# Kernel optimization log

Measured on AMD Instinct MI355X. Metric: run time of the kernel, lower is better.

Reference implementation:

```python
import jax, jax.numpy as jnp
import numpy as np

N = 2048
HW = 36          # resized feature map
NBLK = 4         # n_H = n_V = 4
P = HW // NBLK   # 9x9 patches
C_ENC = 8        # encoder output channels
HD = 2           # ConvLSTM hidden dim
OUT_DIM = 24


def setup_inputs() -> dict:
    key = jax.random.key(0)
    ks = jax.random.split(key, 14)
    s = 0.05
    return {
        "color_feat": jax.random.normal(ks[0], (N, 32, HW, HW), jnp.float32),
        "geo_feat": jax.random.normal(ks[1], (N, 32, HW, HW), jnp.float32),
        # encoder: Conv2d(64,32,1) then Conv2d(32,8,1) -> 1x1 convs as matrices
        "enc_w1": jax.random.normal(ks[2], (32, 64), jnp.float32) * s,
        "enc_b1": jax.random.normal(ks[3], (32,), jnp.float32) * s,
        "enc_w2": jax.random.normal(ks[4], (C_ENC, 32), jnp.float32) * s,
        "enc_b2": jax.random.normal(ks[5], (C_ENC,), jnp.float32) * s,
        # ConvLSTM layer 1: in 8 + hidden 2 -> 4*hidden gates, 1x1 kernel
        "lstm_w1": jax.random.normal(ks[6], (4 * HD, C_ENC + HD), jnp.float32) * s,
        "lstm_b1": jax.random.normal(ks[7], (4 * HD,), jnp.float32) * s,
        # ConvLSTM layer 2: in 2 + hidden 2 -> 4*hidden gates
        "lstm_w2": jax.random.normal(ks[8], (4 * HD, HD + HD), jnp.float32) * s,
        "lstm_b2": jax.random.normal(ks[9], (4 * HD,), jnp.float32) * s,
        # LazyLinear(24) on flattened [N, 2*9*9]
        "out_w": jax.random.normal(ks[10], (OUT_DIM, HD * P * P), jnp.float32) * s,
        "out_b": jax.random.normal(ks[11], (OUT_DIM,), jnp.float32) * s,
    }


def _conv1x1(x, w, b):
    # x: [N,Cin,H,W], w: [Cout,Cin], b: [Cout]
    return jnp.einsum("nchw,oc->nohw", x, w) + b[None, :, None, None]


def _convlstm_layer(x_seq, w, b, hd):
    # x_seq: [T,N,Cin,h,w]; 1x1-kernel ConvLSTM layer, zero-initialized state
    T, n, _, hh, ww = x_seq.shape
    h0 = jnp.zeros((n, hd, hh, ww), x_seq.dtype)
    c0 = jnp.zeros((n, hd, hh, ww), x_seq.dtype)

    def cell(carry, x):
        h, c = carry
        cat = jnp.concatenate([x, h], axis=1)
        gates = jnp.einsum("nchw,gc->nghw", cat, w) + b[None, :, None, None]
        i, f, o, g = jnp.split(gates, 4, axis=1)
        c_next = jax.nn.sigmoid(f) * c + jax.nn.sigmoid(i) * jnp.tanh(g)
        h_next = jax.nn.sigmoid(o) * jnp.tanh(c_next)
        return (h_next, c_next), h_next

    (_, _), h_seq = jax.lax.scan(cell, (h0, c0), x_seq)
    return h_seq  # [T,N,hd,h,w]


def reference(color_feat, geo_feat, enc_w1, enc_b1, enc_w2, enc_b2,
              lstm_w1, lstm_b1, lstm_w2, lstm_b2, out_w, out_b):
    # concat features (already resized to 36x36) -> encoder (two 1x1 convs)
    all_feats = jnp.concatenate([color_feat, geo_feat], axis=1)  # [N,64,36,36]
    enc = _conv1x1(_conv1x1(all_feats, enc_w1, enc_b1), enc_w2, enc_b2)  # [N,8,36,36]

    n = enc.shape[0]
    # torch unfold over (C,H,W) -> [N, 16, C, 9, 9] ordered (h_block, w_block)
    patches = enc.reshape(n, C_ENC, NBLK, P, NBLK, P)
    patches = patches.transpose(0, 2, 4, 1, 3, 5).reshape(n, NBLK * NBLK, C_ENC, P, P)

    x_seq = patches.transpose(1, 0, 2, 3, 4)  # [T=16, N, 8, 9, 9]
    h1 = _convlstm_layer(x_seq, lstm_w1, lstm_b1, HD)   # [T,N,2,9,9]
    h2 = _convlstm_layer(h1, lstm_w2, lstm_b2, HD)      # [T,N,2,9,9]

    last = h2[-1]                       # [N,2,9,9] last timestep of last layer
    flat = last.reshape(n, -1)          # [N,162]
    return flat @ out_w.T + out_b       # [N,24]
```

## Files before the change

### kernel.cpp

```cpp
#include <hip/hip_runtime.h>
#include <cstddef>

#define HWDIM 36
#define PIX   1296
#define PIX4  324
#define CIN   64
#define CENC  8
#define HD    2
#define T_SEQ 16
#define PP    9
#define NPOS  81
#define FLATD 162
#define ODIM  24
#define BLOCK 384

__device__ __forceinline__ float sigm(float x) {
    return 1.f / (1.f + __expf(-x));
}
__device__ __forceinline__ float tanh_f(float x) {
    x = fminf(15.f, fmaxf(-15.f, x));
    float e = __expf(2.f * x);
    return (e - 1.f) / (e + 1.f);
}
__device__ __forceinline__ void fma4(float4& a, float w, const float4& v) {
    a.x = fmaf(w, v.x, a.x);
    a.y = fmaf(w, v.y, a.y);
    a.z = fmaf(w, v.z, a.z);
    a.w = fmaf(w, v.w, a.w);
}

__global__ __launch_bounds__(BLOCK) void lstm_pose_fused(
    const float* __restrict__ color, const float* __restrict__ geo,
    const float* __restrict__ enc_w1, const float* __restrict__ enc_b1,
    const float* __restrict__ enc_w2, const float* __restrict__ enc_b2,
    const float* __restrict__ lw1, const float* __restrict__ lb1,
    const float* __restrict__ lw2, const float* __restrict__ lb2,
    const float* __restrict__ ow, const float* __restrict__ ob,
    float* __restrict__ out)
{
    __shared__ __align__(16) float s_enc[CENC][PIX];
    __shared__ __align__(16) float s_fw[CIN * CENC];
    __shared__ float s_fb[CENC];
    __shared__ float s_w1[80], s_b1[8], s_w2[32], s_b2[8];
    __shared__ float s_flat[FLATD + 2];

    const int t = threadIdx.x;
    const int n = blockIdx.x;

    for (int i = t; i < CIN * CENC; i += BLOCK) {
        const int c = i >> 3, o = i & 7;
        float s = 0.f;
        #pragma unroll
        for (int m = 0; m < 32; ++m)
            s = fmaf(enc_w2[o * 32 + m], enc_w1[m * 64 + c], s);
        s_fw[i] = s;
    }
    if (t < 8) {
        float s = enc_b2[t];
        #pragma unroll
        for (int m = 0; m < 32; ++m)
            s = fmaf(enc_w2[t * 32 + m], enc_b1[m], s);
        s_fb[t] = s;
    }
    if (t >= 64  && t < 144) s_w1[t - 64]  = lw1[t - 64];
    if (t >= 160 && t < 168) s_b1[t - 160] = lb1[t - 160];
    if (t >= 192 && t < 224) s_w2[t - 192] = lw2[t - 192];
    if (t >= 256 && t < 264) s_b2[t - 256] = lb2[t - 256];
    __syncthreads();

    if (t < PIX4) {
        const float4* c4 = reinterpret_cast<const float4*>(color + (size_t)n * 32 * PIX);
        const float4* g4 = reinterpret_cast<const float4*>(geo   + (size_t)n * 32 * PIX);

        float4 acc[8];
        #pragma unroll
        for (int o = 0; o < 8; ++o) {
            const float b = s_fb[o];
            acc[o] = make_float4(b, b, b, b);
        }

        #pragma unroll 8
        for (int cc = 0; cc < 64; ++cc) {
            const int c = cc >> 1;
            const float4 v = (cc & 1) ? g4[c * PIX4 + t] : c4[c * PIX4 + t];
            const int wbase = ((cc & 1) ? (c + 32) : c) * 8;
            const float4 wl = *reinterpret_cast<const float4*>(&s_fw[wbase]);
            const float4 wh = *reinterpret_cast<const float4*>(&s_fw[wbase + 4]);
            fma4(acc[0], wl.x, v); fma4(acc[1], wl.y, v);
            fma4(acc[2], wl.z, v); fma4(acc[3], wl.w, v);
            fma4(acc[4], wh.x, v); fma4(acc[5], wh.y, v);
            fma4(acc[6], wh.z, v); fma4(acc[7], wh.w, v);
        }
        #pragma unroll
        for (int o = 0; o < 8; ++o)
            *reinterpret_cast<float4*>(&s_enc[o][t * 4]) = acc[o];
    }
    __syncthreads();

    if (t < NPOS) {
        const int ph = t / PP, pw = t % PP;
        float h1[2] = {0.f, 0.f}, c1[2] = {0.f, 0.f};
        float h2[2] = {0.f, 0.f}, c2[2] = {0.f, 0.f};

        for (int step = 0; step < T_SEQ; ++step) {
            const int bh = step >> 2, bw = step & 3;
            const int pix = (bh * PP + ph) * HWDIM + (bw * PP + pw);

            float x[CENC];
            #pragma unroll
            for (int c = 0; c < CENC; ++c) x[c] = s_enc[c][pix];

            float g1[8];
            #pragma unroll
            for (int j = 0; j < 8; ++j) {
                float s = s_b1[j];
                #pragma unroll
                for (int c = 0; c < 8; ++c) s = fmaf(s_w1[j * 10 + c], x[c], s);
                s = fmaf(s_w1[j * 10 + 8], h1[0], s);
                s = fmaf(s_w1[j * 10 + 9], h1[1], s);
                g1[j] = s;
            }
            #pragma unroll
            for (int d = 0; d < 2; ++d) {
                const float i_ = sigm(g1[0 + d]);
                const float f_ = sigm(g1[2 + d]);
                const float o_ = sigm(g1[4 + d]);
                const float gg = tanh_f(g1[6 + d]);
                c1[d] = f_ * c1[d] + i_ * gg;
                h1[d] = o_ * tanh_f(c1[d]);
            }

            float g2[8];
            #pragma unroll
            for (int j = 0; j < 8; ++j) {
                float s = s_b2[j];
                s = fmaf(s_w2[j * 4 + 0], h1[0], s);
                s = fmaf(s_w2[j * 4 + 1], h1[1], s);
                s = fmaf(s_w2[j * 4 + 2], h2[0], s);
                s = fmaf(s_w2[j * 4 + 3], h2[1], s);
                g2[j] = s;
            }
            #pragma unroll
            for (int d = 0; d < 2; ++d) {
                const float i_ = sigm(g2[0 + d]);
                const float f_ = sigm(g2[2 + d]);
                const float o_ = sigm(g2[4 + d]);
                const float gg = tanh_f(g2[6 + d]);
                c2[d] = f_ * c2[d] + i_ * gg;
                h2[d] = o_ * tanh_f(c2[d]);
            }
        }
        s_flat[0 * NPOS + t] = h2[0];
        s_flat[1 * NPOS + t] = h2[1];
    }
    __syncthreads();

    if (t < ODIM) {
        float s = ob[t];
        const float* w = ow + t * FLATD;
        #pragma unroll 6
        for (int k = 0; k < FLATD; ++k) s = fmaf(w[k], s_flat[k], s);
        out[(size_t)n * ODIM + t] = s;
    }
}

extern "C" void kernel_launch(void* const* d_in, const int* in_sizes, int n_in,
                              void* d_out, int out_size, void* d_ws, size_t ws_size,
                              hipStream_t stream) {
    const float* color  = (const float*)d_in[0];
    const float* geo    = (const float*)d_in[1];
    const float* enc_w1 = (const float*)d_in[2];
    const float* enc_b1 = (const float*)d_in[3];
    const float* enc_w2 = (const float*)d_in[4];
    const float* enc_b2 = (const float*)d_in[5];
    const float* lw1    = (const float*)d_in[6];
    const float* lb1    = (const float*)d_in[7];
    const float* lw2    = (const float*)d_in[8];
    const float* lb2    = (const float*)d_in[9];
    const float* ow     = (const float*)d_in[10];
    const float* ob     = (const float*)d_in[11];
    float* out = (float*)d_out;

    const int nsamp = in_sizes[0] / (32 * PIX);

    lstm_pose_fused<<<nsamp, BLOCK, 0, stream>>>(
        color, geo, enc_w1, enc_b1, enc_w2, enc_b2,
        lw1, lb1, lw2, lb2, ow, ob, out);
}
```

Measured before the change: 756.0 us.

## Split fused kernel into streaming encoder pass and batched LSTM head kernel

Replaces the single per-sample fused kernel with two kernels when enough workspace exists. The first streams the 1x1 encoder over all pixels in a flat grid of 256-thread blocks and writes the 8-channel encoding to global workspace. The second runs the ConvLSTM recurrence and linear head for four samples per block, using 324 of 384 threads, instead of 81 threads idling the rest of a per-sample block. This removes the serial LSTM tail that blocked bandwidth use in the fused kernel, at the cost of an extra write and read of the encoded tensor and a second launch.

```diff
diff --git a/kernel.cpp b/kernel.cpp
--- a/kernel.cpp
+++ b/kernel.cpp
@@ -6,13 +6,11 @@
 #define PIX4  324
 #define CIN   64
 #define CENC  8
-#define HD    2
 #define T_SEQ 16
 #define PP    9
 #define NPOS  81
 #define FLATD 162
 #define ODIM  24
-#define BLOCK 384
 
 __device__ __forceinline__ float sigm(float x) {
     return 1.f / (1.f + __expf(-x));
@@ -28,6 +26,169 @@
     a.z = fmaf(w, v.z, a.z);
     a.w = fmaf(w, v.w, a.w);
 }
+
+#define K1_BLOCK 256
+
+__global__ __launch_bounds__(K1_BLOCK) void enc_stream(
+    const float* __restrict__ color, const float* __restrict__ geo,
+    const float* __restrict__ enc_w1, const float* __restrict__ enc_b1,
+    const float* __restrict__ enc_w2, const float* __restrict__ enc_b2,
+    float* __restrict__ enc_out, int total4)
+{
+    __shared__ __align__(16) float s_fw[CIN * CENC];
+    __shared__ float s_fb[CENC];
+
+    const int t = threadIdx.x;
+
+    for (int i = t; i < CIN * CENC; i += K1_BLOCK) {
+        const int c = i >> 3, o = i & 7;
+        float s = 0.f;
+        #pragma unroll
+        for (int m = 0; m < 32; ++m)
+            s = fmaf(enc_w2[o * 32 + m], enc_w1[m * 64 + c], s);
+        s_fw[i] = s;
+    }
+    if (t < CENC) {
+        float s = enc_b2[t];
+        #pragma unroll
+        for (int m = 0; m < 32; ++m)
+            s = fmaf(enc_w2[t * 32 + m], enc_b1[m], s);
+        s_fb[t] = s;
+    }
+    __syncthreads();
+
+    const int u = blockIdx.x * K1_BLOCK + t;
+    if (u >= total4) return;
+    const int n = u / PIX4;
+    const int p = u - n * PIX4;
+
+    const float4* c4 = reinterpret_cast<const float4*>(color + (size_t)n * 32 * PIX) + p;
+    const float4* g4 = reinterpret_cast<const float4*>(geo   + (size_t)n * 32 * PIX) + p;
+
+    float4 acc[8];
+    #pragma unroll
+    for (int o = 0; o < 8; ++o) {
+        const float b = s_fb[o];
+        acc[o] = make_float4(b, b, b, b);
+    }
+
+    #pragma unroll 8
+    for (int cc = 0; cc < 64; ++cc) {
+        const int c = cc >> 1;
+        const float4 v = (cc & 1) ? g4[c * PIX4] : c4[c * PIX4];
+        const int wbase = ((cc & 1) ? (c + 32) : c) * 8;
+        const float4 wl = *reinterpret_cast<const float4*>(&s_fw[wbase]);
+        const float4 wh = *reinterpret_cast<const float4*>(&s_fw[wbase + 4]);
+        fma4(acc[0], wl.x, v); fma4(acc[1], wl.y, v);
+        fma4(acc[2], wl.z, v); fma4(acc[3], wl.w, v);
+        fma4(acc[4], wh.x, v); fma4(acc[5], wh.y, v);
+        fma4(acc[6], wh.z, v); fma4(acc[7], wh.w, v);
+    }
+
+    float4* op = reinterpret_cast<float4*>(enc_out + (size_t)n * CENC * PIX);
+    #pragma unroll
+    for (int o = 0; o < 8; ++o)
+        op[o * PIX4 + p] = acc[o];
+}
+
+#define K2_BLOCK 384
+
+__global__ __launch_bounds__(K2_BLOCK) void lstm_head(
+    const float* __restrict__ enc,
+    const float* __restrict__ lw1, const float* __restrict__ lb1,
+    const float* __restrict__ lw2, const float* __restrict__ lb2,
+    const float* __restrict__ ow,  const float* __restrict__ ob,
+    float* __restrict__ out, int nsamp)
+{
+    __shared__ float s_w1[80], s_b1[8], s_w2[32], s_b2[8];
+    __shared__ float s_flat[4][FLATD];
+
+    const int t = threadIdx.x;
+    if (t < 80)       s_w1[t]       = lw1[t];
+    else if (t < 88)  s_b1[t - 80]  = lb1[t - 80];
+    else if (t < 120) s_w2[t - 88]  = lw2[t - 88];
+    else if (t < 128) s_b2[t - 120] = lb2[t - 120];
+    __syncthreads();
+
+    if (t < 4 * NPOS) {
+        const int s   = t / NPOS;
+        const int pos = t - s * NPOS;
+        const int n   = blockIdx.x * 4 + s;
+        if (n < nsamp) {
+            const int ph = pos / PP, pw = pos - ph * PP;
+            const float* ep = enc + (size_t)n * CENC * PIX;
+
+            float h1[2] = {0.f, 0.f}, c1[2] = {0.f, 0.f};
+            float h2[2] = {0.f, 0.f}, c2[2] = {0.f, 0.f};
+
+            for (int step = 0; step < T_SEQ; ++step) {
+                const int bh = step >> 2, bw = step & 3;
+                const int pix = (bh * PP + ph) * HWDIM + (bw * PP + pw);
+
+                float x[CENC];
+                #pragma unroll
+                for (int c = 0; c < CENC; ++c) x[c] = ep[c * PIX + pix];
+
+                float g1[8];
+                #pragma unroll
+                for (int j = 0; j < 8; ++j) {
+                    float s_ = s_b1[j];
+                    #pragma unroll
+                    for (int c = 0; c < 8; ++c) s_ = fmaf(s_w1[j * 10 + c], x[c], s_);
+                    s_ = fmaf(s_w1[j * 10 + 8], h1[0], s_);
+                    s_ = fmaf(s_w1[j * 10 + 9], h1[1], s_);
+                    g1[j] = s_;
+                }
+                #pragma unroll
+                for (int d = 0; d < 2; ++d) {
+                    const float i_ = sigm(g1[0 + d]);
+                    const float f_ = sigm(g1[2 + d]);
+                    const float o_ = sigm(g1[4 + d]);
+                    const float gg = tanh_f(g1[6 + d]);
+                    c1[d] = f_ * c1[d] + i_ * gg;
+                    h1[d] = o_ * tanh_f(c1[d]);
+                }
+
+                float g2[8];
+                #pragma unroll
+                for (int j = 0; j < 8; ++j) {
+                    float s_ = s_b2[j];
+                    s_ = fmaf(s_w2[j * 4 + 0], h1[0], s_);
+                    s_ = fmaf(s_w2[j * 4 + 1], h1[1], s_);
+                    s_ = fmaf(s_w2[j * 4 + 2], h2[0], s_);
+                    s_ = fmaf(s_w2[j * 4 + 3], h2[1], s_);
+                    g2[j] = s_;
+                }
+                #pragma unroll
+                for (int d = 0; d < 2; ++d) {
+                    const float i_ = sigm(g2[0 + d]);
+                    const float f_ = sigm(g2[2 + d]);
+                    const float o_ = sigm(g2[4 + d]);
+                    const float gg = tanh_f(g2[6 + d]);
+                    c2[d] = f_ * c2[d] + i_ * gg;
+                    h2[d] = o_ * tanh_f(c2[d]);
+                }
+            }
+            s_flat[s][pos]        = h2[0];
+            s_flat[s][NPOS + pos] = h2[1];
+        }
+    }
+    __syncthreads();
+
+    if (t < 4 * ODIM) {
+        const int s = t / ODIM, o = t - s * ODIM;
+        const int n = blockIdx.x * 4 + s;
+        if (n < nsamp) {
+            float sum = ob[o];
+            const float* w = ow + o * FLATD;
+            #pragma unroll 6
+            for (int k = 0; k < FLATD; ++k) sum = fmaf(w[k], s_flat[s][k], sum);
+            out[(size_t)n * ODIM + o] = sum;
+        }
+    }
+}
+
+#define BLOCK 384
 
 __global__ __launch_bounds__(BLOCK) void lstm_pose_fused(
     const float* __restrict__ color, const float* __restrict__ geo,
@@ -71,14 +232,12 @@
     if (t < PIX4) {
         const float4* c4 = reinterpret_cast<const float4*>(color + (size_t)n * 32 * PIX);
         const float4* g4 = reinterpret_cast<const float4*>(geo   + (size_t)n * 32 * PIX);
-
         float4 acc[8];
         #pragma unroll
         for (int o = 0; o < 8; ++o) {
             const float b = s_fb[o];
             acc[o] = make_float4(b, b, b, b);
         }
-
         #pragma unroll 8
         for (int cc = 0; cc < 64; ++cc) {
             const int c = cc >> 1;
@@ -101,15 +260,12 @@
         const int ph = t / PP, pw = t % PP;
         float h1[2] = {0.f, 0.f}, c1[2] = {0.f, 0.f};
         float h2[2] = {0.f, 0.f}, c2[2] = {0.f, 0.f};
-
         for (int step = 0; step < T_SEQ; ++step) {
             const int bh = step >> 2, bw = step & 3;
             const int pix = (bh * PP + ph) * HWDIM + (bw * PP + pw);
-
             float x[CENC];
             #pragma unroll
             for (int c = 0; c < CENC; ++c) x[c] = s_enc[c][pix];
-
             float g1[8];
             #pragma unroll
             for (int j = 0; j < 8; ++j) {
@@ -129,7 +285,6 @@
                 c1[d] = f_ * c1[d] + i_ * gg;
                 h1[d] = o_ * tanh_f(c1[d]);
             }
-
             float g2[8];
             #pragma unroll
             for (int j = 0; j < 8; ++j) {
@@ -182,8 +337,20 @@
     float* out = (float*)d_out;
 
     const int nsamp = in_sizes[0] / (32 * PIX);
-
-    lstm_pose_fused<<<nsamp, BLOCK, 0, stream>>>(
-        color, geo, enc_w1, enc_b1, enc_w2, enc_b2,
-        lw1, lb1, lw2, lb2, ow, ob, out);
-}
+    const size_t enc_bytes = (size_t)nsamp * CENC * PIX * sizeof(float);
+
+    if (ws_size >= enc_bytes) {
+        float* enc = (float*)d_ws;
+        const int total4 = nsamp * PIX4;
+        const int g1 = (total4 + K1_BLOCK - 1) / K1_BLOCK;
+        enc_stream<<<g1, K1_BLOCK, 0, stream>>>(
+            color, geo, enc_w1, enc_b1, enc_w2, enc_b2, enc, total4);
+        const int g2 = (nsamp + 3) / 4;
+        lstm_head<<<g2, K2_BLOCK, 0, stream>>>(
+            enc, lw1, lb1, lw2, lb2, ow, ob, out, nsamp);
+    } else {
+        lstm_pose_fused<<<nsamp, BLOCK, 0, stream>>>(
+            color, geo, enc_w1, enc_b1, enc_w2, enc_b2,
+            lw1, lb1, lw2, lb2, ow, ob, out);
+    }
+}
```

Result: no change. 752.3 us (-0.5%).

## Stage encoder inputs through shared memory and shrink the LDS footprint

Applied to the files above, without the earlier changes.

Each block now loads four input channels per round into a shared staging buffer, using all 384 threads with coalesced float4 loads, then accumulates the fused 1x1 encoder from LDS. The staging buffer is then reused to hold encoder outputs in two halves, each laid out per timestep, so the LSTM recurrence runs in two chunks of eight steps. This roughly halves the kernel's shared memory, so more blocks can be resident per CU to hide global-memory latency. The cost is two barriers per round and fewer outstanding loads per thread within a round.

```diff
diff --git a/kernel.cpp b/kernel.cpp
--- a/kernel.cpp
+++ b/kernel.cpp
@@ -6,7 +6,6 @@
 #define PIX4  324
 #define CIN   64
 #define CENC  8
-#define HD    2
 #define T_SEQ 16
 #define PP    9
 #define NPOS  81
@@ -29,7 +28,7 @@
     a.w = fmaf(w, v.w, a.w);
 }
 
-__global__ __launch_bounds__(BLOCK) void lstm_pose_fused(
+__global__ __launch_bounds__(BLOCK) void lstm_pose_v2(
     const float* __restrict__ color, const float* __restrict__ geo,
     const float* __restrict__ enc_w1, const float* __restrict__ enc_b1,
     const float* __restrict__ enc_w2, const float* __restrict__ enc_b2,
@@ -38,11 +37,11 @@
     const float* __restrict__ ow, const float* __restrict__ ob,
     float* __restrict__ out)
 {
-    __shared__ __align__(16) float s_enc[CENC][PIX];
+    __shared__ __align__(16) float s_buf[5184];
     __shared__ __align__(16) float s_fw[CIN * CENC];
     __shared__ float s_fb[CENC];
     __shared__ float s_w1[80], s_b1[8], s_w2[32], s_b2[8];
-    __shared__ float s_flat[FLATD + 2];
+    __shared__ float s_flat[FLATD];
 
     const int t = threadIdx.x;
     const int n = blockIdx.x;
@@ -55,7 +54,7 @@
             s = fmaf(enc_w2[o * 32 + m], enc_w1[m * 64 + c], s);
         s_fw[i] = s;
     }
-    if (t < 8) {
+    if (t < CENC) {
         float s = enc_b2[t];
         #pragma unroll
         for (int m = 0; m < 32; ++m)
@@ -68,90 +67,120 @@
     if (t >= 256 && t < 264) s_b2[t - 256] = lb2[t - 256];
     __syncthreads();
 
-    if (t < PIX4) {
-        const float4* c4 = reinterpret_cast<const float4*>(color + (size_t)n * 32 * PIX);
-        const float4* g4 = reinterpret_cast<const float4*>(geo   + (size_t)n * 32 * PIX);
-
-        float4 acc[8];
-        #pragma unroll
-        for (int o = 0; o < 8; ++o) {
-            const float b = s_fb[o];
-            acc[o] = make_float4(b, b, b, b);
-        }
-
-        #pragma unroll 8
-        for (int cc = 0; cc < 64; ++cc) {
-            const int c = cc >> 1;
-            const float4 v = (cc & 1) ? g4[c * PIX4 + t] : c4[c * PIX4 + t];
-            const int wbase = ((cc & 1) ? (c + 32) : c) * 8;
-            const float4 wl = *reinterpret_cast<const float4*>(&s_fw[wbase]);
-            const float4 wh = *reinterpret_cast<const float4*>(&s_fw[wbase + 4]);
-            fma4(acc[0], wl.x, v); fma4(acc[1], wl.y, v);
-            fma4(acc[2], wl.z, v); fma4(acc[3], wl.w, v);
-            fma4(acc[4], wh.x, v); fma4(acc[5], wh.y, v);
-            fma4(acc[6], wh.z, v); fma4(acc[7], wh.w, v);
-        }
-        #pragma unroll
-        for (int o = 0; o < 8; ++o)
-            *reinterpret_cast<float4*>(&s_enc[o][t * 4]) = acc[o];
-    }
-    __syncthreads();
-
-    if (t < NPOS) {
-        const int ph = t / PP, pw = t % PP;
-        float h1[2] = {0.f, 0.f}, c1[2] = {0.f, 0.f};
-        float h2[2] = {0.f, 0.f}, c2[2] = {0.f, 0.f};
-
-        for (int step = 0; step < T_SEQ; ++step) {
-            const int bh = step >> 2, bw = step & 3;
-            const int pix = (bh * PP + ph) * HWDIM + (bw * PP + pw);
-
-            float x[CENC];
+    float4 acc[8];
+    #pragma unroll
+    for (int o = 0; o < 8; ++o) {
+        const float b = s_fb[o];
+        acc[o] = make_float4(b, b, b, b);
+    }
+
+    const float4* csrc = reinterpret_cast<const float4*>(color + (size_t)n * 32 * PIX);
+    const float4* gsrc = reinterpret_cast<const float4*>(geo   + (size_t)n * 32 * PIX);
+    float4* st4 = reinterpret_cast<float4*>(s_buf);
+
+    for (int r = 0; r < 16; ++r) {
+        const float4* src = (r < 8) ? (csrc + r * 1296) : (gsrc + (r - 8) * 1296);
+        st4[t]        = src[t];
+        st4[t + 384]  = src[t + 384];
+        st4[t + 768]  = src[t + 768];
+        if (t < 144) st4[t + 1152] = src[t + 1152];
+        __syncthreads();
+        if (t < PIX4) {
             #pragma unroll
-            for (int c = 0; c < CENC; ++c) x[c] = s_enc[c][pix];
-
-            float g1[8];
-            #pragma unroll
-            for (int j = 0; j < 8; ++j) {
-                float s = s_b1[j];
-                #pragma unroll
-                for (int c = 0; c < 8; ++c) s = fmaf(s_w1[j * 10 + c], x[c], s);
-                s = fmaf(s_w1[j * 10 + 8], h1[0], s);
-                s = fmaf(s_w1[j * 10 + 9], h1[1], s);
-                g1[j] = s;
-            }
-            #pragma unroll
-            for (int d = 0; d < 2; ++d) {
-                const float i_ = sigm(g1[0 + d]);
-                const float f_ = sigm(g1[2 + d]);
-                const float o_ = sigm(g1[4 + d]);
-                const float gg = tanh_f(g1[6 + d]);
-                c1[d] = f_ * c1[d] + i_ * gg;
-                h1[d] = o_ * tanh_f(c1[d]);
-            }
-
-            float g2[8];
-            #pragma unroll
-            for (int j = 0; j < 8; ++j) {
-                float s = s_b2[j];
-                s = fmaf(s_w2[j * 4 + 0], h1[0], s);
-                s = fmaf(s_w2[j * 4 + 1], h1[1], s);
-                s = fmaf(s_w2[j * 4 + 2], h2[0], s);
-                s = fmaf(s_w2[j * 4 + 3], h2[1], s);
-                g2[j] = s;
-            }
-            #pragma unroll
-            for (int d = 0; d < 2; ++d) {
-                const float i_ = sigm(g2[0 + d]);
-                const float f_ = sigm(g2[2 + d]);
-                const float o_ = sigm(g2[4 + d]);
-                const float gg = tanh_f(g2[6 + d]);
-                c2[d] = f_ * c2[d] + i_ * gg;
-                h2[d] = o_ * tanh_f(c2[d]);
+            for (int k = 0; k < 4; ++k) {
+                const float4 v = st4[k * PIX4 + t];
+                const int c = r * 4 + k;
+                const float4 wl = *reinterpret_cast<const float4*>(&s_fw[c * 8]);
+                const float4 wh = *reinterpret_cast<const float4*>(&s_fw[c * 8 + 4]);
+                fma4(acc[0], wl.x, v); fma4(acc[1], wl.y, v);
+                fma4(acc[2], wl.z, v); fma4(acc[3], wl.w, v);
+                fma4(acc[4], wh.x, v); fma4(acc[5], wh.y, v);
+                fma4(acc[6], wh.z, v); fma4(acc[7], wh.w, v);
             }
         }
-        s_flat[0 * NPOS + t] = h2[0];
-        s_flat[1 * NPOS + t] = h2[1];
+        __syncthreads();
+    }
+
+    float h1[2] = {0.f, 0.f}, c1[2] = {0.f, 0.f};
+    float h2[2] = {0.f, 0.f}, c2[2] = {0.f, 0.f};
+
+    for (int cidx = 0; cidx < 2; ++cidx) {
+        if (t < PIX4) {
+            const int hh = t / 9;
+            const int bh = hh / 9;
+            if ((bh >> 1) == cidx) {
+                const int ph = hh % 9;
+                const int w0 = (t % 9) * 4;
+                #pragma unroll
+                for (int j = 0; j < 4; ++j) {
+                    const int w   = w0 + j;
+                    const int stl = (bh & 1) * 4 + (w / 9);
+                    const int pos = ph * 9 + (w % 9);
+                    const int base = stl * 648 + pos;
+                    #pragma unroll
+                    for (int c = 0; c < 8; ++c) {
+                        const float4 a = acc[c];
+                        const float v = (j == 0) ? a.x : (j == 1) ? a.y : (j == 2) ? a.z : a.w;
+                        s_buf[base + c * 81] = v;
+                    }
+                }
+            }
+        }
+        __syncthreads();
+
+        if (t < NPOS) {
+            for (int stl = 0; stl < 8; ++stl) {
+                float x[CENC];
+                #pragma unroll
+                for (int c = 0; c < 8; ++c) x[c] = s_buf[stl * 648 + c * 81 + t];
+
+                float g1[8];
+                #pragma unroll
+                for (int j = 0; j < 8; ++j) {
+                    float s = s_b1[j];
+                    #pragma unroll
+                    for (int c = 0; c < 8; ++c) s = fmaf(s_w1[j * 10 + c], x[c], s);
+                    s = fmaf(s_w1[j * 10 + 8], h1[0], s);
+                    s = fmaf(s_w1[j * 10 + 9], h1[1], s);
+                    g1[j] = s;
+                }
+                #pragma unroll
+                for (int d = 0; d < 2; ++d) {
+                    const float i_ = sigm(g1[0 + d]);
+                    const float f_ = sigm(g1[2 + d]);
+                    const float o_ = sigm(g1[4 + d]);
+                    const float gg = tanh_f(g1[6 + d]);
+                    c1[d] = f_ * c1[d] + i_ * gg;
+                    h1[d] = o_ * tanh_f(c1[d]);
+                }
+
+                float g2[8];
+                #pragma unroll
+                for (int j = 0; j < 8; ++j) {
+                    float s = s_b2[j];
+                    s = fmaf(s_w2[j * 4 + 0], h1[0], s);
+                    s = fmaf(s_w2[j * 4 + 1], h1[1], s);
+                    s = fmaf(s_w2[j * 4 + 2], h2[0], s);
+                    s = fmaf(s_w2[j * 4 + 3], h2[1], s);
+                    g2[j] = s;
+                }
+                #pragma unroll
+                for (int d = 0; d < 2; ++d) {
+                    const float i_ = sigm(g2[0 + d]);
+                    const float f_ = sigm(g2[2 + d]);
+                    const float o_ = sigm(g2[4 + d]);
+                    const float gg = tanh_f(g2[6 + d]);
+                    c2[d] = f_ * c2[d] + i_ * gg;
+                    h2[d] = o_ * tanh_f(c2[d]);
+                }
+            }
+        }
+        __syncthreads();
+    }
+
+    if (t < NPOS) {
+        s_flat[t]        = h2[0];
+        s_flat[NPOS + t] = h2[1];
     }
     __syncthreads();
 
@@ -183,7 +212,7 @@
 
     const int nsamp = in_sizes[0] / (32 * PIX);
 
-    lstm_pose_fused<<<nsamp, BLOCK, 0, stream>>>(
+    lstm_pose_v2<<<nsamp, BLOCK, 0, stream>>>(
         color, geo, enc_w1, enc_b1, enc_w2, enc_b2,
         lw1, lb1, lw2, lb2, ow, ob, out);
 }
```

Result: slower. 901.0 us (+19.2%).
